# Optimization experiments

Hardware: AMD Instinct MI355X
Metric: run time of the kernel (lower is better)

## Reference

```python
import jax, jax.numpy as jnp
import numpy as np
import math

K = 20        # args.k  (global-branch neighbors)
KL = 20       # args.kl (local-branch neighbors)
EPS = 1e-5    # BatchNorm eps
SLOPE = 0.2   # LeakyReLU slope


def _knn(x, k, keep):
    # x: [B,C,N]; keep: [B,N] bool column mask. pd = -||xi - xj||^2.
    xx = jnp.sum(x * x, axis=1)                          # [B,N]
    inner = jnp.einsum('bci,bcj->bij', x, x)             # [B,N,N]
    pd = 2.0 * inner - xx[:, :, None] - xx[:, None, :]
    mn = jnp.min(pd, axis=-1)                            # per-row min
    # suppressed columns are set to the row min so topk never selects them
    pd = jnp.where(keep[:, None, :], pd, mn[:, :, None])
    return jax.lax.top_k(pd, k)[1]                       # [B,N,k]


def _gather(pts, idx):
    # pts: [B,N,C], idx: [B,N,k] -> [B,N,k,C]
    b = jnp.arange(pts.shape[0])[:, None, None]
    return pts[b, idx]


def _edge_feat(x, k, keep, smooth):
    # DGCNN edge features: concat(neighbor - center, center) -> [B,2C,N,k]
    idx = _knn(x, k, keep)
    xp = jnp.transpose(x, (0, 2, 1))                     # [B,N,C]
    if smooth:
        # GraphLayer: neighbors come from a topk-mean smoothed field
        knn_x = _gather(xp, idx)                         # [B,N,k,C]
        k2 = math.ceil(k * 2 / 3)
        top = jax.lax.top_k(jnp.transpose(knn_x, (0, 1, 3, 2)), k2)[0]
        src = jnp.mean(top, axis=-1)                     # [B,N,C]
    else:
        src = xp
    feat = _gather(src, idx)                             # [B,N,k,C]
    ctr = jnp.broadcast_to(xp[:, :, None, :], feat.shape)
    out = jnp.concatenate([feat - ctr, ctr], axis=-1)    # [B,N,k,2C]
    return jnp.transpose(out, (0, 3, 1, 2))


def _bn(y, axes):
    # BatchNorm (training-mode batch stats, gamma=1, beta=0 as at init)
    mu = jnp.mean(y, axis=axes, keepdims=True)
    var = jnp.var(y, axis=axes, keepdims=True)
    return (y - mu) * jax.lax.rsqrt(var + EPS)


def _conv_block(x, w, axes):
    # 1x1 conv (no bias) + BN + LeakyReLU
    ein = 'oc,bcnk->bonk' if x.ndim == 4 else 'oc,bcn->bon'
    return jax.nn.leaky_relu(_bn(jnp.einsum(ein, w, x), axes), SLOPE)


def _forward(x, local_idx, w1, w2, w3, w4, w5, w6, w7, w8, w9,
             l1w, l2w, l2b, l3w, l3b):
    keep_l = local_idx
    keep_g = jnp.logical_not(local_idx)
    ax4 = (0, 2, 3)
    # local (smoothed GraphLayer) branch, neighbors restricted to local points
    xl1 = _conv_block(_edge_feat(x,   KL, keep_l, True), w1, ax4).max(-1)
    xl2 = _conv_block(_edge_feat(xl1, KL, keep_l, True), w2, ax4).max(-1)
    xl3 = _conv_block(_edge_feat(xl2, KL, keep_l, True), w3, ax4).max(-1)
    xl4 = _conv_block(_edge_feat(xl3, KL, keep_l, True), w4, ax4).max(-1)
    x_local = jnp.concatenate([xl1, xl2, xl3, xl4], axis=1)  # [B,512,N]
    # global branch, neighbors restricted to non-local points
    xg1 = _conv_block(_edge_feat(x,   K, keep_g, False), w5, ax4).max(-1)
    xg2 = _conv_block(_edge_feat(xg1, K, keep_g, False), w6, ax4).max(-1)
    xg3 = _conv_block(_edge_feat(xg2, K, keep_g, False), w7, ax4).max(-1)
    xg4 = _conv_block(_edge_feat(xg3, K, keep_g, False), w8, ax4).max(-1)
    x_glob = jnp.concatenate([xg1, xg2, xg3, xg4], axis=1)   # [B,512,N]
    # per-point merge: local columns take the local-branch features
    h = jnp.where(local_idx[:, None, :], x_local, x_glob)
    h = _conv_block(h, w9, (0, 2))                            # [B,E,N]
    g = jnp.concatenate([h.max(-1), h.mean(-1)], axis=1)      # [B,2E]
    # head: linears + BN1d + LeakyReLU; dropout is identity (eval mode)
    g = jax.nn.leaky_relu(_bn(g @ l1w.T, (0,)), SLOPE)
    g = jax.nn.leaky_relu(_bn(g @ l2w.T + l2b, (0,)), SLOPE)
    return g @ l3w.T + l3b


def setup_inputs() -> dict:
    key = jax.random.key(0)
    ks = jax.random.split(key, 16)
    B, N, E, OUT = 4, 2048, 1024, 40

    def w(k, o, i):
        return jax.random.normal(k, (o, i), jnp.float32) / np.sqrt(i)

    return {
        'x': jax.random.normal(ks[0], (B, 3, N), jnp.float32),
        'local_idx': jax.random.bernoulli(ks[1], 0.5, (B, N)),
        'geod_dist': jax.random.normal(ks[2], (B, N), jnp.float32),
        'w1': w(ks[3], 64, 6),   'w2': w(ks[4], 64, 128),
        'w3': w(ks[5], 128, 128), 'w4': w(ks[6], 256, 256),
        'w5': w(ks[7], 64, 6),   'w6': w(ks[8], 64, 128),
        'w7': w(ks[9], 128, 128), 'w8': w(ks[10], 256, 256),
        'w9': w(ks[11], E, 512),
        'l1w': w(ks[12], 512, 2 * E),
        'l2w': w(ks[13], 256, 512),
        'l2b': jnp.zeros((256,), jnp.float32),
        'l3w': w(ks[14], OUT, 256),
        'l3b': jnp.zeros((OUT,), jnp.float32),
    }


def reference(x, local_idx, geod_dist, w1, w2, w3, w4, w5, w6, w7, w8, w9,
              l1w, l2w, l2b, l3w, l3b):
    del geod_dist  # accepted but unused in the original forward
    return _forward(x, local_idx, w1, w2, w3, w4, w5, w6, w7, w8, w9,
                    l1w, l2w, l2b, l3w, l3b)
```

## Files before the change

kernel.cpp:

```cpp
#include <hip/hip_runtime.h>
#include <hip/hip_bf16.h>
#include <cfloat>

#define BB 4
#define NN 2048
#define KNN 20
#define KTOP 14
#define EPSBN 1e-5f
#define SLOPE 0.2f

__global__ void k_xx3(const float* __restrict__ x, float* __restrict__ xx) {
  int t = blockIdx.x * 64 + threadIdx.x;
  int b = t >> 11, n = t & 2047;
  const float* xb = x + (long)b * (3L * NN) + n;
  float v0 = xb[0], v1 = xb[NN], v2 = xb[2 * NN];
  xx[t] = v0 * v0 + v1 * v1 + v2 * v2;
}

__device__ __forceinline__ void suppress(float* __restrict__ trow,
                                         const int* __restrict__ lrow,
                                         int keepv, int lane) {
  int base = 4 * lane;
#pragma unroll
  for (int q = 0; q < 8; ++q) {
    float4 lv = *(const float4*)(trow + 256 * q + base);
    int4 kv = *(const int4*)(lrow + 256 * q + base);
    lv.x = (((kv.x != 0) ? 1 : 0) == keepv) ? lv.x : -FLT_MAX;
    lv.y = (((kv.y != 0) ? 1 : 0) == keepv) ? lv.y : -FLT_MAX;
    lv.z = (((kv.z != 0) ? 1 : 0) == keepv) ? lv.z : -FLT_MAX;
    lv.w = (((kv.w != 0) ? 1 : 0) == keepv) ? lv.w : -FLT_MAX;
    *(float4*)(trow + 256 * q + base) = lv;
  }
}

__device__ __forceinline__ void sel_lds(float* __restrict__ trow, int lane,
                                        int* __restrict__ orow) {
  int base = 4 * lane;
  for (int t = 0; t < KNN; ++t) {
    float v[32];
#pragma unroll
    for (int q = 0; q < 8; ++q) {
      float4 lv = *(const float4*)(trow + 256 * q + base);
      v[4 * q + 0] = lv.x; v[4 * q + 1] = lv.y;
      v[4 * q + 2] = lv.z; v[4 * q + 3] = lv.w;
    }
    float mv[16]; int mi[16];
#pragma unroll
    for (int s = 0; s < 16; ++s) {
      mi[s] = (v[2 * s] >= v[2 * s + 1]) ? 2 * s : 2 * s + 1;
      mv[s] = fmaxf(v[2 * s], v[2 * s + 1]);
    }
#pragma unroll
    for (int s = 0; s < 8; ++s) {
      mi[s] = (mv[2 * s] >= mv[2 * s + 1]) ? mi[2 * s] : mi[2 * s + 1];
      mv[s] = fmaxf(mv[2 * s], mv[2 * s + 1]);
    }
#pragma unroll
    for (int s = 0; s < 4; ++s) {
      mi[s] = (mv[2 * s] >= mv[2 * s + 1]) ? mi[2 * s] : mi[2 * s + 1];
      mv[s] = fmaxf(mv[2 * s], mv[2 * s + 1]);
    }
    int i01 = (mv[0] >= mv[1]) ? mi[0] : mi[1];
    float v01 = fmaxf(mv[0], mv[1]);
    int i23 = (mv[2] >= mv[3]) ? mi[2] : mi[3];
    float v23 = fmaxf(mv[2], mv[3]);
    int li = (v01 >= v23) ? i01 : i23;
    float bv = fmaxf(v01, v23);
    float gv = bv;
#pragma unroll
    for (int d = 1; d < 64; d <<= 1) gv = fmaxf(gv, __shfl_xor(gv, d));
    unsigned long long mk = __ballot(bv == gv);
    int wl = (int)(__ffsll((long long)mk) - 1);
    int jloc = 256 * (li >> 2) + base + (li & 3);
    int bj = __shfl(jloc, wl);
    if (lane == 0) { orow[t] = bj; trow[bj] = -FLT_MAX; }
  }
}

template <int C, int DUAL>
__global__ __launch_bounds__(256) void k_knn(
    const float* __restrict__ xbase, long bstride, const float* __restrict__ xxbase,
    const int* __restrict__ lidx, int keepv,
    int* __restrict__ idxA, int* __restrict__ idxB ) {
  __shared__ float tile[4][NN];
  __shared__ float a_lds[C][4];
  int b = blockIdx.y;
  int i0 = blockIdx.x * 4;
  const float* xb = xbase + (long)b * bstride;
  const float* xxb = xxbase + b * NN;
  int tid = threadIdx.x, wid = tid >> 6, lane = tid & 63;
  for (int t = tid; t < 4 * C; t += 256) {
    int c = t >> 2, r = t & 3;
    a_lds[c][r] = xb[(long)c * NN + i0 + r];
  }
  __syncthreads();
  const int* lrow = lidx + b * NN;
  int i = i0 + wid;
  for (int pass = 0; pass < 1 + DUAL; ++pass) {
    if (pass) __syncthreads();
    for (int jt = 0; jt < NN; jt += 1024) {
      float acc[4][4];
#pragma unroll
      for (int r = 0; r < 4; ++r)
#pragma unroll
        for (int s = 0; s < 4; ++s) acc[r][s] = 0.f;
#pragma unroll 4
      for (int c = 0; c < C; ++c) {
        float4 a = *(const float4*)&a_lds[c][0];
        float4 h = *(const float4*)&xb[(long)c * NN + jt + tid * 4];
        acc[0][0] += a.x * h.x; acc[0][1] += a.x * h.y; acc[0][2] += a.x * h.z; acc[0][3] += a.x * h.w;
        acc[1][0] += a.y * h.x; acc[1][1] += a.y * h.y; acc[1][2] += a.y * h.z; acc[1][3] += a.y * h.w;
        acc[2][0] += a.z * h.x; acc[2][1] += a.z * h.y; acc[2][2] += a.z * h.z; acc[2][3] += a.z * h.w;
        acc[3][0] += a.w * h.x; acc[3][1] += a.w * h.y; acc[3][2] += a.w * h.z; acc[3][3] += a.w * h.w;
      }
      float4 xxj = *(const float4*)&xxb[jt + tid * 4];
#pragma unroll
      for (int r = 0; r < 4; ++r) {
        float xxi = xxb[i0 + r];
        float4 o;
        o.x = 2.f * acc[r][0] - xxi - xxj.x;
        o.y = 2.f * acc[r][1] - xxi - xxj.y;
        o.z = 2.f * acc[r][2] - xxi - xxj.z;
        o.w = 2.f * acc[r][3] - xxi - xxj.w;
        *(float4*)&tile[r][jt + tid * 4] = o;
      }
    }
    __syncthreads();
    float* trow = &tile[wid][0];
    int kvp = pass ? (1 - keepv) : keepv;
    int* ob = pass ? idxB : idxA;
    suppress(trow, lrow, kvp, lane);
    sel_lds(trow, lane, ob + ((long)b * NN + i) * KNN);
  }
}

__global__ void k_smooth(const float* __restrict__ x, long bstride, int C,
                         const int* __restrict__ idx, float* __restrict__ src) {
  long t = (long)blockIdx.x * blockDim.x + threadIdx.x;
  if (t >= (long)BB * C * NN) return;
  int n = (int)(t % NN);
  int c = (int)((t / NN) % C);
  int b = (int)(t / ((long)NN * C));
  const int* id = idx + ((long)b * NN + n) * KNN;
  const float* xb = x + (long)b * bstride + (long)c * NN;
  float v[KNN]; float sum = 0.f;
#pragma unroll
  for (int kk = 0; kk < KNN; ++kk) { v[kk] = xb[id[kk]]; sum += v[kk]; }
  int r0 = -1, r1 = -1, r2 = -1, r3 = -1, r4 = -1, r5 = -1;
#pragma unroll
  for (int r = 0; r < KNN - KTOP; ++r) {
    float mvv = FLT_MAX; int mi = -1;
#pragma unroll
    for (int j = 0; j < KNN; ++j) {
      if (j == r0 || j == r1 || j == r2 || j == r3 || j == r4 || j == r5) continue;
      if (v[j] < mvv) { mvv = v[j]; mi = j; }
    }
    sum -= mvv;
    if (r == 0) r0 = mi; else if (r == 1) r1 = mi; else if (r == 2) r2 = mi;
    else if (r == 3) r3 = mi; else if (r == 4) r4 = mi; else r5 = mi;
  }
  src[((long)b * C + c) * NN + n] = sum * (1.f / KTOP);
}

__global__ void k_wprep_all(
    const float* __restrict__ w1, const float* __restrict__ w2,
    const float* __restrict__ w3, const float* __restrict__ w4,
    const float* __restrict__ w5, const float* __restrict__ w6,
    const float* __restrict__ w7, const float* __restrict__ w8,
    float* __restrict__ wa, float* __restrict__ wd) {
  int L = blockIdx.y;
  const float* w; int O, C; long off;
  switch (L) {
    case 0: w = w1; O = 64;  C = 3;   off = 0;     break;
    case 1: w = w2; O = 64;  C = 64;  off = 192;   break;
    case 2: w = w3; O = 128; C = 64;  off = 4288;  break;
    case 3: w = w4; O = 256; C = 128; off = 12480; break;
    case 4: w = w5; O = 64;  C = 3;   off = 45248; break;
    case 5: w = w6; O = 64;  C = 64;  off = 45440; break;
    case 6: w = w7; O = 128; C = 64;  off = 49536; break;
    default: w = w8; O = 256; C = 128; off = 57728; break;
  }
  for (int t = blockIdx.x * blockDim.x + threadIdx.x; t < O * C;
       t += gridDim.x * blockDim.x) {
    int o = t / C, c = t % C;
    float a = w[(long)o * 2 * C + c];
    float bb = w[(long)o * 2 * C + C + c];
    wa[off + (long)c * O + o] = a;
    wd[off + (long)c * O + o] = bb - a;
  }
}

template <int C>
__global__ __launch_bounds__(256) void k_zt2(
    const float* __restrict__ Ma, long mas,
    const float* __restrict__ Mb_, long mbs,
    const float* __restrict__ wa, const float* __restrict__ wd,
    int O, float* __restrict__ Zs, float* __restrict__ Zd) {
  constexpr int KC = (C >= 16) ? 16 : C;
  __shared__ float As[KC][64], Bs[KC][64];
  int z = blockIdx.z;
  int nyo = gridDim.y >> 1;
  int half = (blockIdx.y >= nyo) ? 1 : 0;
  int o0 = (half ? (blockIdx.y - nyo) : blockIdx.y) * 64;
  const float* M = half ? Mb_ : Ma;
  long ms = half ? mbs : mas;
  const float* Wt = half ? wd : wa;
  float* T = half ? Zd : Zs;
  const float* Mb = M + (long)z * ms;
  float* Tb = T + (long)z * NN * O;
  int tid = threadIdx.x;
  int tx = tid & 15, ty = tid >> 4;
  int n0 = blockIdx.x * 64;
  float acc[4][4];
#pragma unroll
  for (int r = 0; r < 4; ++r)
#pragma unroll
    for (int s = 0; s < 4; ++s) acc[r][s] = 0.f;
  for (int c0 = 0; c0 < C; c0 += KC) {
    for (int e = tid; e < KC * 64; e += 256) {
      int c = e >> 6, ii = e & 63;
      As[c][ii] = Mb[(long)(c0 + c) * NN + n0 + ii];
      Bs[c][ii] = Wt[(long)(c0 + c) * O + o0 + ii];
    }
    __syncthreads();
#pragma unroll
    for (int cc = 0; cc < KC; ++cc) {
      float4 a = *(const float4*)&As[cc][ty * 4];
      float4 h = *(const float4*)&Bs[cc][tx * 4];
      acc[0][0] += a.x * h.x; acc[0][1] += a.x * h.y; acc[0][2] += a.x * h.z; acc[0][3] += a.x * h.w;
      acc[1][0] += a.y * h.x; acc[1][1] += a.y * h.y; acc[1][2] += a.y * h.z; acc[1][3] += a.y * h.w;
      acc[2][0] += a.z * h.x; acc[2][1] += a.z * h.y; acc[2][2] += a.z * h.z; acc[2][3] += a.z * h.w;
      acc[3][0] += a.w * h.x; acc[3][1] += a.w * h.y; acc[3][2] += a.w * h.z; acc[3][3] += a.w * h.w;
    }
    __syncthreads();
  }
#pragma unroll
  for (int r = 0; r < 4; ++r) {
    float4 v; v.x = acc[r][0]; v.y = acc[r][1]; v.z = acc[r][2]; v.w = acc[r][3];
    *(float4*)&Tb[(long)(n0 + ty * 4 + r) * O + o0 + tx * 4] = v;
  }
}

template <int O, int PTS>
__global__ __launch_bounds__(O) void k_gmax(
    const float* __restrict__ Zs, const float* __restrict__ Zd,
    const int* __restrict__ idx, float* __restrict__ ymax,
    float* __restrict__ stats) {
  int tid = threadIdx.x;
  int bn0 = blockIdx.x * PTS;
  int b = bn0 >> 11;
  long zbase = (long)b * NN * O;
  float ss = 0.f, sq = 0.f;
  for (int p = 0; p < PTS; ++p) {
    int bn = bn0 + p;
    const int* ir = idx + (long)bn * KNN;
    float zd = Zd[(long)bn * O + tid];
    float smax = -FLT_MAX;
#pragma unroll
    for (int k = 0; k < KNN; ++k) {
      float y = Zs[zbase + (long)ir[k] * O + tid] + zd;
      smax = fmaxf(smax, y); ss += y; sq += y * y;
    }
    ymax[(long)bn * O + tid] = smax;
  }
  atomicAdd(&stats[tid], ss);
  atomicAdd(&stats[O + tid], sq);
}

__global__ void k_bnmax(const float* __restrict__ ymax, const float* __restrict__ stats,
                        int O, float invcnt, float* __restrict__ out, long out_bstride,
                        float* __restrict__ xxout) {
  long t = (long)blockIdx.x * blockDim.x + threadIdx.x;
  if (t >= (long)BB * O * NN) return;
  int n = (int)(t % NN);
  int o = (int)((t / NN) % O);
  int b = (int)(t / ((long)NN * O));
  float mu = stats[o] * invcnt;
  float var = stats[O + o] * invcnt - mu * mu;
  float rs = rsqrtf(var + EPSBN);
  float v = (ymax[((long)b * NN + n) * O + o] - mu) * rs;
  v = v >= 0.f ? v : SLOPE * v;
  out[(long)b * out_bstride + (long)o * NN + n] = v;
  if (xxout) atomicAdd(&xxout[b * NN + n], v * v);
}

__global__ __launch_bounds__(256) void k_gemm9(
    const float* __restrict__ W, const float* __restrict__ xl,
    const float* __restrict__ xg, const int* __restrict__ lidx,
    float* __restrict__ h2, float* __restrict__ stats) {
  __shared__ float Ws[16][68];
  __shared__ float Hs[16][68];
  int tid = threadIdx.x;
  int tx = tid & 15, ty = tid >> 4;
  int p0 = blockIdx.x * 64, o0 = blockIdx.y * 64;
  int b = p0 >> 11, n0 = p0 & 2047;
  int hp = tid & 63, cq = (tid >> 6) * 4;
  const float* hbase;
  {
    int pt = p0 + hp;
    hbase = (lidx[pt] ? xl : xg) + (long)b * (512L * NN) + (pt & 2047);
  }
  int wo = tid >> 2, wc = (tid & 3) * 4;
  float acc[4][4];
#pragma unroll
  for (int i = 0; i < 4; ++i)
#pragma unroll
    for (int j = 0; j < 4; ++j) acc[i][j] = 0.f;

  for (int c0 = 0; c0 < 512; c0 += 16) {
    float4 wv = *(const float4*)(W + (long)(o0 + wo) * 512 + c0 + wc);
    Ws[wc + 0][wo] = wv.x; Ws[wc + 1][wo] = wv.y;
    Ws[wc + 2][wo] = wv.z; Ws[wc + 3][wo] = wv.w;
    long crow = (long)(c0 + cq) * NN;
    Hs[cq + 0][hp] = hbase[crow];
    Hs[cq + 1][hp] = hbase[crow + NN];
    Hs[cq + 2][hp] = hbase[crow + 2 * NN];
    Hs[cq + 3][hp] = hbase[crow + 3 * NN];
    __syncthreads();
#pragma unroll
    for (int cc = 0; cc < 16; ++cc) {
      float4 a = *(const float4*)&Ws[cc][ty * 4];
      float4 h = *(const float4*)&Hs[cc][tx * 4];
      acc[0][0] += a.x * h.x; acc[0][1] += a.x * h.y; acc[0][2] += a.x * h.z; acc[0][3] += a.x * h.w;
      acc[1][0] += a.y * h.x; acc[1][1] += a.y * h.y; acc[1][2] += a.y * h.z; acc[1][3] += a.y * h.w;
      acc[2][0] += a.z * h.x; acc[2][1] += a.z * h.y; acc[2][2] += a.z * h.z; acc[2][3] += a.z * h.w;
      acc[3][0] += a.w * h.x; acc[3][1] += a.w * h.y; acc[3][2] += a.w * h.z; acc[3][3] += a.w * h.w;
    }
    __syncthreads();
  }
#pragma unroll
  for (int i = 0; i < 4; ++i) {
    int o = o0 + ty * 4 + i;
    float4 v; v.x = acc[i][0]; v.y = acc[i][1]; v.z = acc[i][2]; v.w = acc[i][3];
    *(float4*)&h2[((long)b * 1024 + o) * NN + n0 + tx * 4] = v;
    float ss = acc[i][0] + acc[i][1] + acc[i][2] + acc[i][3];
    float sq = acc[i][0] * acc[i][0] + acc[i][1] * acc[i][1] +
               acc[i][2] * acc[i][2] + acc[i][3] * acc[i][3];
    for (int d = 8; d > 0; d >>= 1) {
      ss += __shfl_down(ss, d, 16);
      sq += __shfl_down(sq, d, 16);
    }
    if (tx == 0) {
      atomicAdd(&stats[o], ss);
      atomicAdd(&stats[1024 + o], sq);
    }
  }
}

__global__ void k_gpool(const float* __restrict__ h2, const float* __restrict__ stats,
                        float* __restrict__ g) {
  int b = blockIdx.x / 1024, o = blockIdx.x % 1024;
  int tid = threadIdx.x;
  float mu = stats[o] * (1.f / 8192.f);
  float var = stats[1024 + o] * (1.f / 8192.f) - mu * mu;
  float rs = rsqrtf(var + EPSBN);
  const float* hr = h2 + ((long)b * 1024 + o) * NN;
  float mx = -FLT_MAX, sm = 0.f;
  for (int n = tid; n < NN; n += 256) {
    float v = (hr[n] - mu) * rs; v = v >= 0.f ? v : SLOPE * v;
    mx = fmaxf(mx, v); sm += v;
  }
  __shared__ float smx[256], ssm[256];
  smx[tid] = mx; ssm[tid] = sm; __syncthreads();
  for (int s = 128; s > 0; s >>= 1) {
    if (tid < s) { smx[tid] = fmaxf(smx[tid], smx[tid + s]); ssm[tid] += ssm[tid + s]; }
    __syncthreads();
  }
  if (tid == 0) { g[b * 2048 + o] = smx[0]; g[b * 2048 + 1024 + o] = ssm[0] * (1.f / NN); }
}

__global__ void k_head(const float* __restrict__ gin, int CIN, const float* __restrict__ wl,
                       const float* __restrict__ bias, float* __restrict__ gout, int do_bn) {
  int f = blockIdx.x, tid = threadIdx.x, F = gridDim.x;
  const float* wr = wl + (long)f * CIN;
  float a0 = 0, a1 = 0, a2 = 0, a3 = 0;
  for (int c = tid; c < CIN; c += 256) {
    float wv = wr[c];
    a0 += wv * gin[c];         a1 += wv * gin[CIN + c];
    a2 += wv * gin[2 * CIN + c]; a3 += wv * gin[3 * CIN + c];
  }
  __shared__ float s0[256], s1[256], s2[256], s3[256];
  s0[tid] = a0; s1[tid] = a1; s2[tid] = a2; s3[tid] = a3; __syncthreads();
  for (int s = 128; s > 0; s >>= 1) {
    if (tid < s) { s0[tid] += s0[tid + s]; s1[tid] += s1[tid + s];
                   s2[tid] += s2[tid + s]; s3[tid] += s3[tid + s]; }
    __syncthreads();
  }
  if (tid == 0) {
    float z0 = s0[0], z1 = s1[0], z2 = s2[0], z3 = s3[0];
    if (bias) { float bb = bias[f]; z0 += bb; z1 += bb; z2 += bb; z3 += bb; }
    if (do_bn) {
      float mu = 0.25f * (z0 + z1 + z2 + z3);
      float var = 0.25f * (z0 * z0 + z1 * z1 + z2 * z2 + z3 * z3) - mu * mu;
      float rs = rsqrtf(var + EPSBN);
      z0 = (z0 - mu) * rs; z1 = (z1 - mu) * rs; z2 = (z2 - mu) * rs; z3 = (z3 - mu) * rs;
      z0 = z0 >= 0.f ? z0 : SLOPE * z0; z1 = z1 >= 0.f ? z1 : SLOPE * z1;
      z2 = z2 >= 0.f ? z2 : SLOPE * z2; z3 = z3 >= 0.f ? z3 : SLOPE * z3;
    }
    gout[0 * F + f] = z0; gout[1 * F + f] = z1; gout[2 * F + f] = z2; gout[3 * F + f] = z3;
  }
}

extern "C" void kernel_launch(void* const* d_in, const int* in_sizes, int n_in,
                              void* d_out, int out_size, void* d_ws, size_t ws_size,
                              hipStream_t stream) {
  const float* x   = (const float*)d_in[0];
  const int*   lidx= (const int*)d_in[1];
  const float* w1  = (const float*)d_in[3];
  const float* w2  = (const float*)d_in[4];
  const float* w3  = (const float*)d_in[5];
  const float* w4  = (const float*)d_in[6];
  const float* w5  = (const float*)d_in[7];
  const float* w6  = (const float*)d_in[8];
  const float* w7  = (const float*)d_in[9];
  const float* w8  = (const float*)d_in[10];
  const float* w9  = (const float*)d_in[11];
  const float* l1w = (const float*)d_in[12];
  const float* l2w = (const float*)d_in[13];
  const float* l2b = (const float*)d_in[14];
  const float* l3w = (const float*)d_in[15];
  const float* l3b = (const float*)d_in[16];
  float* out = (float*)d_out;

  float* ws    = (float*)d_ws;
  float* xxall = ws;
  float* stats = ws + 57344;
  int*   idxb  = (int*)(ws + 61440);
  float* xloc  = ws + 225280;
  float* xglb  = ws + 4419584;
  float* big   = ws + 8613888;
  float* g     = ws + 17002496;
  float* g1    = ws + 17010688;
  float* g2    = ws + 17012736;
  float* waall = ws + 17013760;
  float* wdall = ws + 17104256;

  float* srcb  = big;
  float* Zs    = big + 1048576;
  float* Zd    = big + 3145728;
  float* ymaxb = big + 5242880;
  float* h2    = big;
  int*   idxG  = (int*)xglb;

  float* xxS0 = xxall;
  float* xxS1 = xxall + 8192;
  float* xxS2 = xxall + 16384;
  float* xxS3 = xxall + 24576;
  float* xxS4 = xxall + 32768;
  float* xxS5 = xxall + 40960;
  float* xxS6 = xxall + 49152;

  float* SL1 = stats + 0;    float* SL2 = stats + 128;
  float* SL3 = stats + 256;  float* SL4 = stats + 512;
  float* SG1 = stats + 1024; float* SG2 = stats + 1152;
  float* SG3 = stats + 1280; float* SG4 = stats + 1536;
  float* S9  = stats + 2048;

  const float invE = 1.f / (BB * NN * KNN);
  const long XS0 = 3L * NN;
  const long XS  = 512L * NN;
  const dim3 gknn(NN / 4, BB);

  hipMemsetAsync(ws, 0, 61440 * sizeof(float), stream);
  k_wprep_all<<<dim3(128, 8), 256, 0, stream>>>(w1, w2, w3, w4, w5, w6, w7, w8,
                                                waall, wdall);
  k_xx3<<<128, 64, 0, stream>>>(x, xxS0);

  k_knn<3, 1><<<gknn, 256, 0, stream>>>(x, XS0, xxS0, lidx, 1, idxb, idxG);

  k_smooth<<<(BB * 3 * NN + 255) / 256, 256, 0, stream>>>(x, XS0, 3, idxb, srcb);
  k_zt2<3><<<dim3(32, 2, 4), 256, 0, stream>>>(srcb, 3L * NN, x, XS0,
                                               waall + 0, wdall + 0, 64, Zs, Zd);
  k_gmax<64, 8><<<BB * NN / 8, 64, 0, stream>>>(Zs, Zd, idxb, ymaxb, SL1);
  k_bnmax<<<(BB * 64 * NN + 255) / 256, 256, 0, stream>>>(ymaxb, SL1, 64, invE,
                                                          xloc + 0 * NN, XS, xxS1);
  k_knn<64, 0><<<gknn, 256, 0, stream>>>(xloc, XS, xxS1, lidx, 1, idxb, nullptr);
  k_smooth<<<(BB * 64 * NN + 255) / 256, 256, 0, stream>>>(xloc, XS, 64, idxb, srcb);
  k_zt2<64><<<dim3(32, 2, 4), 256, 0, stream>>>(srcb, 64L * NN, xloc, XS,
                                                waall + 192, wdall + 192, 64, Zs, Zd);
  k_gmax<64, 8><<<BB * NN / 8, 64, 0, stream>>>(Zs, Zd, idxb, ymaxb, SL2);
  k_bnmax<<<(BB * 64 * NN + 255) / 256, 256, 0, stream>>>(ymaxb, SL2, 64, invE,
                                                          xloc + 64 * NN, XS, xxS2);
  k_knn<64, 0><<<gknn, 256, 0, stream>>>(xloc + 64 * NN, XS, xxS2, lidx, 1, idxb, nullptr);
  k_smooth<<<(BB * 64 * NN + 255) / 256, 256, 0, stream>>>(xloc + 64 * NN, XS, 64, idxb, srcb);
  k_zt2<64><<<dim3(32, 4, 4), 256, 0, stream>>>(srcb, 64L * NN, xloc + 64 * NN, XS,
                                                waall + 4288, wdall + 4288, 128, Zs, Zd);
  k_gmax<128, 16><<<BB * NN / 16, 128, 0, stream>>>(Zs, Zd, idxb, ymaxb, SL3);
  k_bnmax<<<(BB * 128 * NN + 255) / 256, 256, 0, stream>>>(ymaxb, SL3, 128, invE,
                                                           xloc + 128 * NN, XS, xxS3);
  k_knn<128, 0><<<gknn, 256, 0, stream>>>(xloc + 128 * NN, XS, xxS3, lidx, 1, idxb, nullptr);
  k_smooth<<<(BB * 128 * NN + 255) / 256, 256, 0, stream>>>(xloc + 128 * NN, XS, 128, idxb, srcb);
  k_zt2<128><<<dim3(32, 8, 4), 256, 0, stream>>>(srcb, 128L * NN, xloc + 128 * NN, XS,
                                                 waall + 12480, wdall + 12480, 256, Zs, Zd);
  k_gmax<256, 16><<<BB * NN / 16, 256, 0, stream>>>(Zs, Zd, idxb, ymaxb, SL4);
  k_bnmax<<<(BB * 256 * NN + 255) / 256, 256, 0, stream>>>(ymaxb, SL4, 256, invE,
                                                           xloc + 256 * NN, XS, nullptr);

  k_zt2<3><<<dim3(32, 2, 4), 256, 0, stream>>>(x, XS0, x, XS0,
                                               waall + 45248, wdall + 45248, 64, Zs, Zd);
  k_gmax<64, 8><<<BB * NN / 8, 64, 0, stream>>>(Zs, Zd, idxG, ymaxb, SG1);
  k_bnmax<<<(BB * 64 * NN + 255) / 256, 256, 0, stream>>>(ymaxb, SG1, 64, invE,
                                                          xglb + 0 * NN, XS, xxS4);
  k_knn<64, 0><<<gknn, 256, 0, stream>>>(xglb, XS, xxS4, lidx, 0, idxb, nullptr);
  k_zt2<64><<<dim3(32, 2, 4), 256, 0, stream>>>(xglb, XS, xglb, XS,
                                                waall + 45440, wdall + 45440, 64, Zs, Zd);
  k_gmax<64, 8><<<BB * NN / 8, 64, 0, stream>>>(Zs, Zd, idxb, ymaxb, SG2);
  k_bnmax<<<(BB * 64 * NN + 255) / 256, 256, 0, stream>>>(ymaxb, SG2, 64, invE,
                                                          xglb + 64 * NN, XS, xxS5);
  k_knn<64, 0><<<gknn, 256, 0, stream>>>(xglb + 64 * NN, XS, xxS5, lidx, 0, idxb, nullptr);
  k_zt2<64><<<dim3(32, 4, 4), 256, 0, stream>>>(xglb + 64 * NN, XS, xglb + 64 * NN, XS,
                                                waall + 49536, wdall + 49536, 128, Zs, Zd);
  k_gmax<128, 16><<<BB * NN / 16, 128, 0, stream>>>(Zs, Zd, idxb, ymaxb, SG3);
  k_bnmax<<<(BB * 128 * NN + 255) / 256, 256, 0, stream>>>(ymaxb, SG3, 128, invE,
                                                           xglb + 128 * NN, XS, xxS6);
  k_knn<128, 0><<<gknn, 256, 0, stream>>>(xglb + 128 * NN, XS, xxS6, lidx, 0, idxb, nullptr);
  k_zt2<128><<<dim3(32, 8, 4), 256, 0, stream>>>(xglb + 128 * NN, XS, xglb + 128 * NN, XS,
                                                 waall + 57728, wdall + 57728, 256, Zs, Zd);
  k_gmax<256, 16><<<BB * NN / 16, 256, 0, stream>>>(Zs, Zd, idxb, ymaxb, SG4);
  k_bnmax<<<(BB * 256 * NN + 255) / 256, 256, 0, stream>>>(ymaxb, SG4, 256, invE,
                                                           xglb + 256 * NN, XS, nullptr);

  {
    dim3 g9(NN * BB / 64, 1024 / 64);
    k_gemm9<<<g9, 256, 0, stream>>>(w9, xloc, xglb, lidx, h2, S9);
  }
  k_gpool<<<BB * 1024, 256, 0, stream>>>(h2, S9, g);
  k_head<<<512, 256, 0, stream>>>(g, 2048, l1w, nullptr, g1, 1);
  k_head<<<256, 256, 0, stream>>>(g1, 512, l2w, l2b, g2, 1);
  k_head<<<40, 256, 0, stream>>>(g2, 256, l3w, l3b, out, 0);
}
```

Before: 1.272 ms.

## Interleave local and global branches to batch kNN launches, widen gemm9 tile

The local and global DGCNN branches are now interleaved so that each pair of same-width kNN searches runs in one launch, with a z-dimension selecting the branch. This doubles the grid size of each kNN launch, fills more CUs, and removes three launches. A separate global index buffer is added so the two branches do not overwrite each other's indices. Independently, the final 512->1024 GEMM tile grows from 64x64 to 64x128 points with 8x4 accumulators per thread, raising register use in exchange for more reuse.

```diff
diff --git a/kernel.cpp b/kernel.cpp
--- a/kernel.cpp
+++ b/kernel.cpp
@@ -77,11 +77,50 @@
   }
 }
 
-template <int C, int DUAL>
-__global__ __launch_bounds__(256) void k_knn(
+template <int C>
+__device__ __forceinline__ void knn_body(
+    float (*tile)[NN], float (*a_lds)[4],
+    const float* __restrict__ xb, const float* __restrict__ xxb,
+    const int* __restrict__ lrow, int i0, int keepv,
+    int* __restrict__ orowbase, int tid, int wid, int lane) {
+  for (int jt = 0; jt < NN; jt += 1024) {
+    float acc[4][4];
+#pragma unroll
+    for (int r = 0; r < 4; ++r)
+#pragma unroll
+      for (int s = 0; s < 4; ++s) acc[r][s] = 0.f;
+#pragma unroll 4
+    for (int c = 0; c < C; ++c) {
+      float4 a = *(const float4*)&a_lds[c][0];
+      float4 h = *(const float4*)&xb[(long)c * NN + jt + tid * 4];
+      acc[0][0] += a.x * h.x; acc[0][1] += a.x * h.y; acc[0][2] += a.x * h.z; acc[0][3] += a.x * h.w;
+      acc[1][0] += a.y * h.x; acc[1][1] += a.y * h.y; acc[1][2] += a.y * h.z; acc[1][3] += a.y * h.w;
+      acc[2][0] += a.z * h.x; acc[2][1] += a.z * h.y; acc[2][2] += a.z * h.z; acc[2][3] += a.z * h.w;
+      acc[3][0] += a.w * h.x; acc[3][1] += a.w * h.y; acc[3][2] += a.w * h.z; acc[3][3] += a.w * h.w;
+    }
+    float4 xxj = *(const float4*)&xxb[jt + tid * 4];
+#pragma unroll
+    for (int r = 0; r < 4; ++r) {
+      float xxi = xxb[i0 + r];
+      float4 o;
+      o.x = 2.f * acc[r][0] - xxi - xxj.x;
+      o.y = 2.f * acc[r][1] - xxi - xxj.y;
+      o.z = 2.f * acc[r][2] - xxi - xxj.z;
+      o.w = 2.f * acc[r][3] - xxi - xxj.w;
+      *(float4*)&tile[r][jt + tid * 4] = o;
+    }
+  }
+  __syncthreads();
+  float* trow = &tile[wid][0];
+  suppress(trow, lrow, keepv, lane);
+  sel_lds(trow, lane, orowbase);
+}
+
+template <int C>
+__global__ __launch_bounds__(256) void k_knn_dual(
     const float* __restrict__ xbase, long bstride, const float* __restrict__ xxbase,
-    const int* __restrict__ lidx, int keepv,
-    int* __restrict__ idxA, int* __restrict__ idxB ) {
+    const int* __restrict__ lidx,
+    int* __restrict__ idxA , int* __restrict__ idxB ) {
   __shared__ float tile[4][NN];
   __shared__ float a_lds[C][4];
   int b = blockIdx.y;
@@ -96,42 +135,40 @@
   __syncthreads();
   const int* lrow = lidx + b * NN;
   int i = i0 + wid;
-  for (int pass = 0; pass < 1 + DUAL; ++pass) {
-    if (pass) __syncthreads();
-    for (int jt = 0; jt < NN; jt += 1024) {
-      float acc[4][4];
-#pragma unroll
-      for (int r = 0; r < 4; ++r)
-#pragma unroll
-        for (int s = 0; s < 4; ++s) acc[r][s] = 0.f;
-#pragma unroll 4
-      for (int c = 0; c < C; ++c) {
-        float4 a = *(const float4*)&a_lds[c][0];
-        float4 h = *(const float4*)&xb[(long)c * NN + jt + tid * 4];
-        acc[0][0] += a.x * h.x; acc[0][1] += a.x * h.y; acc[0][2] += a.x * h.z; acc[0][3] += a.x * h.w;
-        acc[1][0] += a.y * h.x; acc[1][1] += a.y * h.y; acc[1][2] += a.y * h.z; acc[1][3] += a.y * h.w;
-        acc[2][0] += a.z * h.x; acc[2][1] += a.z * h.y; acc[2][2] += a.z * h.z; acc[2][3] += a.z * h.w;
-        acc[3][0] += a.w * h.x; acc[3][1] += a.w * h.y; acc[3][2] += a.w * h.z; acc[3][3] += a.w * h.w;
-      }
-      float4 xxj = *(const float4*)&xxb[jt + tid * 4];
-#pragma unroll
-      for (int r = 0; r < 4; ++r) {
-        float xxi = xxb[i0 + r];
-        float4 o;
-        o.x = 2.f * acc[r][0] - xxi - xxj.x;
-        o.y = 2.f * acc[r][1] - xxi - xxj.y;
-        o.z = 2.f * acc[r][2] - xxi - xxj.z;
-        o.w = 2.f * acc[r][3] - xxi - xxj.w;
-        *(float4*)&tile[r][jt + tid * 4] = o;
-      }
-    }
-    __syncthreads();
-    float* trow = &tile[wid][0];
-    int kvp = pass ? (1 - keepv) : keepv;
-    int* ob = pass ? idxB : idxA;
-    suppress(trow, lrow, kvp, lane);
-    sel_lds(trow, lane, ob + ((long)b * NN + i) * KNN);
-  }
+  knn_body<C>(tile, a_lds, xb, xxb, lrow, i0, 1,
+              idxA + ((long)b * NN + i) * KNN, tid, wid, lane);
+  __syncthreads();
+  knn_body<C>(tile, a_lds, xb, xxb, lrow, i0, 0,
+              idxB + ((long)b * NN + i) * KNN, tid, wid, lane);
+}
+
+template <int C>
+__global__ __launch_bounds__(256) void k_knn2(
+    const float* __restrict__ xA, const float* __restrict__ xxA,
+    int* __restrict__ idxA,
+    const float* __restrict__ xB, const float* __restrict__ xxB,
+    int* __restrict__ idxB, long bstride, const int* __restrict__ lidx) {
+  __shared__ float tile[4][NN];
+  __shared__ float a_lds[C][4];
+  int half = blockIdx.z;
+  const float* xbase = half ? xB : xA;
+  const float* xxbase = half ? xxB : xxA;
+  int keepv = half ? 0 : 1;
+  int* idxO = half ? idxB : idxA;
+  int b = blockIdx.y;
+  int i0 = blockIdx.x * 4;
+  const float* xb = xbase + (long)b * bstride;
+  const float* xxb = xxbase + b * NN;
+  int tid = threadIdx.x, wid = tid >> 6, lane = tid & 63;
+  for (int t = tid; t < 4 * C; t += 256) {
+    int c = t >> 2, r = t & 3;
+    a_lds[c][r] = xb[(long)c * NN + i0 + r];
+  }
+  __syncthreads();
+  const int* lrow = lidx + b * NN;
+  int i = i0 + wid;
+  knn_body<C>(tile, a_lds, xb, xxb, lrow, i0, keepv,
+              idxO + ((long)b * NN + i) * KNN, tid, wid, lane);
 }
 
 __global__ void k_smooth(const float* __restrict__ x, long bstride, int C,
@@ -288,22 +325,22 @@
     const float* __restrict__ W, const float* __restrict__ xl,
     const float* __restrict__ xg, const int* __restrict__ lidx,
     float* __restrict__ h2, float* __restrict__ stats) {
-  __shared__ float Ws[16][68];
-  __shared__ float Hs[16][68];
+  __shared__ float Ws[16][72];
+  __shared__ float Hs[16][132];
   int tid = threadIdx.x;
-  int tx = tid & 15, ty = tid >> 4;
-  int p0 = blockIdx.x * 64, o0 = blockIdx.y * 64;
+  int tx = tid & 31, ty = tid >> 5;
+  int p0 = blockIdx.x * 128, o0 = blockIdx.y * 64;
   int b = p0 >> 11, n0 = p0 & 2047;
-  int hp = tid & 63, cq = (tid >> 6) * 4;
+  int sp = tid & 127, scq = (tid >> 7) * 8;
   const float* hbase;
   {
-    int pt = p0 + hp;
+    int pt = p0 + sp;
     hbase = (lidx[pt] ? xl : xg) + (long)b * (512L * NN) + (pt & 2047);
   }
   int wo = tid >> 2, wc = (tid & 3) * 4;
-  float acc[4][4];
-#pragma unroll
-  for (int i = 0; i < 4; ++i)
+  float acc[8][4];
+#pragma unroll
+  for (int i = 0; i < 8; ++i)
 #pragma unroll
     for (int j = 0; j < 4; ++j) acc[i][j] = 0.f;
 
@@ -311,34 +348,37 @@
     float4 wv = *(const float4*)(W + (long)(o0 + wo) * 512 + c0 + wc);
     Ws[wc + 0][wo] = wv.x; Ws[wc + 1][wo] = wv.y;
     Ws[wc + 2][wo] = wv.z; Ws[wc + 3][wo] = wv.w;
-    long crow = (long)(c0 + cq) * NN;
-    Hs[cq + 0][hp] = hbase[crow];
-    Hs[cq + 1][hp] = hbase[crow + NN];
-    Hs[cq + 2][hp] = hbase[crow + 2 * NN];
-    Hs[cq + 3][hp] = hbase[crow + 3 * NN];
+    long crow = (long)(c0 + scq) * NN;
+#pragma unroll
+    for (int e = 0; e < 8; ++e) Hs[scq + e][sp] = hbase[crow + (long)e * NN];
     __syncthreads();
 #pragma unroll
     for (int cc = 0; cc < 16; ++cc) {
-      float4 a = *(const float4*)&Ws[cc][ty * 4];
+      float4 a0 = *(const float4*)&Ws[cc][ty * 8];
+      float4 a1 = *(const float4*)&Ws[cc][ty * 8 + 4];
       float4 h = *(const float4*)&Hs[cc][tx * 4];
-      acc[0][0] += a.x * h.x; acc[0][1] += a.x * h.y; acc[0][2] += a.x * h.z; acc[0][3] += a.x * h.w;
-      acc[1][0] += a.y * h.x; acc[1][1] += a.y * h.y; acc[1][2] += a.y * h.z; acc[1][3] += a.y * h.w;
-      acc[2][0] += a.z * h.x; acc[2][1] += a.z * h.y; acc[2][2] += a.z * h.z; acc[2][3] += a.z * h.w;
-      acc[3][0] += a.w * h.x; acc[3][1] += a.w * h.y; acc[3][2] += a.w * h.z; acc[3][3] += a.w * h.w;
+      acc[0][0] += a0.x * h.x; acc[0][1] += a0.x * h.y; acc[0][2] += a0.x * h.z; acc[0][3] += a0.x * h.w;
+      acc[1][0] += a0.y * h.x; acc[1][1] += a0.y * h.y; acc[1][2] += a0.y * h.z; acc[1][3] += a0.y * h.w;
+      acc[2][0] += a0.z * h.x; acc[2][1] += a0.z * h.y; acc[2][2] += a0.z * h.z; acc[2][3] += a0.z * h.w;
+      acc[3][0] += a0.w * h.x; acc[3][1] += a0.w * h.y; acc[3][2] += a0.w * h.z; acc[3][3] += a0.w * h.w;
+      acc[4][0] += a1.x * h.x; acc[4][1] += a1.x * h.y; acc[4][2] += a1.x * h.z; acc[4][3] += a1.x * h.w;
+      acc[5][0] += a1.y * h.x; acc[5][1] += a1.y * h.y; acc[5][2] += a1.y * h.z; acc[5][3] += a1.y * h.w;
+      acc[6][0] += a1.z * h.x; acc[6][1] += a1.z * h.y; acc[6][2] += a1.z * h.z; acc[6][3] += a1.z * h.w;
+      acc[7][0] += a1.w * h.x; acc[7][1] += a1.w * h.y; acc[7][2] += a1.w * h.z; acc[7][3] += a1.w * h.w;
     }
     __syncthreads();
   }
 #pragma unroll
-  for (int i = 0; i < 4; ++i) {
-    int o = o0 + ty * 4 + i;
+  for (int i = 0; i < 8; ++i) {
+    int o = o0 + ty * 8 + i;
     float4 v; v.x = acc[i][0]; v.y = acc[i][1]; v.z = acc[i][2]; v.w = acc[i][3];
     *(float4*)&h2[((long)b * 1024 + o) * NN + n0 + tx * 4] = v;
     float ss = acc[i][0] + acc[i][1] + acc[i][2] + acc[i][3];
     float sq = acc[i][0] * acc[i][0] + acc[i][1] * acc[i][1] +
                acc[i][2] * acc[i][2] + acc[i][3] * acc[i][3];
-    for (int d = 8; d > 0; d >>= 1) {
-      ss += __shfl_down(ss, d, 16);
-      sq += __shfl_down(sq, d, 16);
+    for (int d = 16; d > 0; d >>= 1) {
+      ss += __shfl_down(ss, d, 32);
+      sq += __shfl_down(sq, d, 32);
     }
     if (tx == 0) {
       atomicAdd(&stats[o], ss);
@@ -439,6 +479,7 @@
   float* Zs    = big + 1048576;
   float* Zd    = big + 3145728;
   float* ymaxb = big + 5242880;
+  int*   idxG2 = (int*)(big + 7340032);
   float* h2    = big;
   int*   idxG  = (int*)xglb;
 
@@ -460,13 +501,14 @@
   const long XS0 = 3L * NN;
   const long XS  = 512L * NN;
   const dim3 gknn(NN / 4, BB);
+  const dim3 gknn2(NN / 4, BB, 2);
 
   hipMemsetAsync(ws, 0, 61440 * sizeof(float), stream);
   k_wprep_all<<<dim3(128, 8), 256, 0, stream>>>(w1, w2, w3, w4, w5, w6, w7, w8,
                                                 waall, wdall);
   k_xx3<<<128, 64, 0, stream>>>(x, xxS0);
 
-  k_knn<3, 1><<<gknn, 256, 0, stream>>>(x, XS0, xxS0, lidx, 1, idxb, idxG);
+  k_knn_dual<3><<<gknn, 256, 0, stream>>>(x, XS0, xxS0, lidx, idxb, idxG);
 
   k_smooth<<<(BB * 3 * NN + 255) / 256, 256, 0, stream>>>(x, XS0, 3, idxb, srcb);
   k_zt2<3><<<dim3(32, 2, 4), 256, 0, stream>>>(srcb, 3L * NN, x, XS0,
@@ -474,54 +516,56 @@
   k_gmax<64, 8><<<BB * NN / 8, 64, 0, stream>>>(Zs, Zd, idxb, ymaxb, SL1);
   k_bnmax<<<(BB * 64 * NN + 255) / 256, 256, 0, stream>>>(ymaxb, SL1, 64, invE,
                                                           xloc + 0 * NN, XS, xxS1);
-  k_knn<64, 0><<<gknn, 256, 0, stream>>>(xloc, XS, xxS1, lidx, 1, idxb, nullptr);
+  k_zt2<3><<<dim3(32, 2, 4), 256, 0, stream>>>(x, XS0, x, XS0,
+                                               waall + 45248, wdall + 45248, 64, Zs, Zd);
+  k_gmax<64, 8><<<BB * NN / 8, 64, 0, stream>>>(Zs, Zd, idxG, ymaxb, SG1);
+  k_bnmax<<<(BB * 64 * NN + 255) / 256, 256, 0, stream>>>(ymaxb, SG1, 64, invE,
+                                                          xglb + 0 * NN, XS, xxS4);
+
+  k_knn2<64><<<gknn2, 256, 0, stream>>>(xloc, xxS1, idxb,
+                                        xglb, xxS4, idxG2, XS, lidx);
   k_smooth<<<(BB * 64 * NN + 255) / 256, 256, 0, stream>>>(xloc, XS, 64, idxb, srcb);
   k_zt2<64><<<dim3(32, 2, 4), 256, 0, stream>>>(srcb, 64L * NN, xloc, XS,
                                                 waall + 192, wdall + 192, 64, Zs, Zd);
   k_gmax<64, 8><<<BB * NN / 8, 64, 0, stream>>>(Zs, Zd, idxb, ymaxb, SL2);
   k_bnmax<<<(BB * 64 * NN + 255) / 256, 256, 0, stream>>>(ymaxb, SL2, 64, invE,
                                                           xloc + 64 * NN, XS, xxS2);
-  k_knn<64, 0><<<gknn, 256, 0, stream>>>(xloc + 64 * NN, XS, xxS2, lidx, 1, idxb, nullptr);
+  k_zt2<64><<<dim3(32, 2, 4), 256, 0, stream>>>(xglb, XS, xglb, XS,
+                                                waall + 45440, wdall + 45440, 64, Zs, Zd);
+  k_gmax<64, 8><<<BB * NN / 8, 64, 0, stream>>>(Zs, Zd, idxG2, ymaxb, SG2);
+  k_bnmax<<<(BB * 64 * NN + 255) / 256, 256, 0, stream>>>(ymaxb, SG2, 64, invE,
+                                                          xglb + 64 * NN, XS, xxS5);
+
+  k_knn2<64><<<gknn2, 256, 0, stream>>>(xloc + 64 * NN, xxS2, idxb,
+                                        xglb + 64 * NN, xxS5, idxG2, XS, lidx);
   k_smooth<<<(BB * 64 * NN + 255) / 256, 256, 0, stream>>>(xloc + 64 * NN, XS, 64, idxb, srcb);
   k_zt2<64><<<dim3(32, 4, 4), 256, 0, stream>>>(srcb, 64L * NN, xloc + 64 * NN, XS,
                                                 waall + 4288, wdall + 4288, 128, Zs, Zd);
   k_gmax<128, 16><<<BB * NN / 16, 128, 0, stream>>>(Zs, Zd, idxb, ymaxb, SL3);
   k_bnmax<<<(BB * 128 * NN + 255) / 256, 256, 0, stream>>>(ymaxb, SL3, 128, invE,
                                                            xloc + 128 * NN, XS, xxS3);
-  k_knn<128, 0><<<gknn, 256, 0, stream>>>(xloc + 128 * NN, XS, xxS3, lidx, 1, idxb, nullptr);
+  k_zt2<64><<<dim3(32, 4, 4), 256, 0, stream>>>(xglb + 64 * NN, XS, xglb + 64 * NN, XS,
+                                                waall + 49536, wdall + 49536, 128, Zs, Zd);
+  k_gmax<128, 16><<<BB * NN / 16, 128, 0, stream>>>(Zs, Zd, idxG2, ymaxb, SG3);
+  k_bnmax<<<(BB * 128 * NN + 255) / 256, 256, 0, stream>>>(ymaxb, SG3, 128, invE,
+                                                           xglb + 128 * NN, XS, xxS6);
+
+  k_knn2<128><<<gknn2, 256, 0, stream>>>(xloc + 128 * NN, xxS3, idxb,
+                                         xglb + 128 * NN, xxS6, idxG2, XS, lidx);
   k_smooth<<<(BB * 128 * NN + 255) / 256, 256, 0, stream>>>(xloc + 128 * NN, XS, 128, idxb, srcb);
   k_zt2<128><<<dim3(32, 8, 4), 256, 0, stream>>>(srcb, 128L * NN, xloc + 128 * NN, XS,
                                                  waall + 12480, wdall + 12480, 256, Zs, Zd);
   k_gmax<256, 16><<<BB * NN / 16, 256, 0, stream>>>(Zs, Zd, idxb, ymaxb, SL4);
   k_bnmax<<<(BB * 256 * NN + 255) / 256, 256, 0, stream>>>(ymaxb, SL4, 256, invE,
                                                            xloc + 256 * NN, XS, nullptr);
-
-  k_zt2<3><<<dim3(32, 2, 4), 256, 0, stream>>>(x, XS0, x, XS0,
-                                               waall + 45248, wdall + 45248, 64, Zs, Zd);
-  k_gmax<64, 8><<<BB * NN / 8, 64, 0, stream>>>(Zs, Zd, idxG, ymaxb, SG1);
-  k_bnmax<<<(BB * 64 * NN + 255) / 256, 256, 0, stream>>>(ymaxb, SG1, 64, invE,
-                                                          xglb + 0 * NN, XS, xxS4);
-  k_knn<64, 0><<<gknn, 256, 0, stream>>>(xglb, XS, xxS4, lidx, 0, idxb, nullptr);
-  k_zt2<64><<<dim3(32, 2, 4), 256, 0, stream>>>(xglb, XS, xglb, XS,
-                                                waall + 45440, wdall + 45440, 64, Zs, Zd);
-  k_gmax<64, 8><<<BB * NN / 8, 64, 0, stream>>>(Zs, Zd, idxb, ymaxb, SG2);
-  k_bnmax<<<(BB * 64 * NN + 255) / 256, 256, 0, stream>>>(ymaxb, SG2, 64, invE,
-                                                          xglb + 64 * NN, XS, xxS5);
-  k_knn<64, 0><<<gknn, 256, 0, stream>>>(xglb + 64 * NN, XS, xxS5, lidx, 0, idxb, nullptr);
-  k_zt2<64><<<dim3(32, 4, 4), 256, 0, stream>>>(xglb + 64 * NN, XS, xglb + 64 * NN, XS,
-                                                waall + 49536, wdall + 49536, 128, Zs, Zd);
-  k_gmax<128, 16><<<BB * NN / 16, 128, 0, stream>>>(Zs, Zd, idxb, ymaxb, SG3);
-  k_bnmax<<<(BB * 128 * NN + 255) / 256, 256, 0, stream>>>(ymaxb, SG3, 128, invE,
-                                                           xglb + 128 * NN, XS, xxS6);
-  k_knn<128, 0><<<gknn, 256, 0, stream>>>(xglb + 128 * NN, XS, xxS6, lidx, 0, idxb, nullptr);
   k_zt2<128><<<dim3(32, 8, 4), 256, 0, stream>>>(xglb + 128 * NN, XS, xglb + 128 * NN, XS,
                                                  waall + 57728, wdall + 57728, 256, Zs, Zd);
-  k_gmax<256, 16><<<BB * NN / 16, 256, 0, stream>>>(Zs, Zd, idxb, ymaxb, SG4);
+  k_gmax<256, 16><<<BB * NN / 16, 256, 0, stream>>>(Zs, Zd, idxG2, ymaxb, SG4);
   k_bnmax<<<(BB * 256 * NN + 255) / 256, 256, 0, stream>>>(ymaxb, SG4, 256, invE,
                                                            xglb + 256 * NN, XS, nullptr);
 
   {
-    dim3 g9(NN * BB / 64, 1024 / 64);
+    dim3 g9(NN * BB / 128, 1024 / 64);
     k_gemm9<<<g9, 256, 0, stream>>>(w9, xloc, xglb, lidx, h2, S9);
   }
   k_gpool<<<BB * 1024, 256, 0, stream>>>(h2, S9, g);
```

Result: faster. 1.219 ms (-4.2%).
